# Kernel tuning notes

Measured on AMD Instinct MI355X. Metric: run time of the kernel, lower is better.

## Reference

```python
import jax, jax.numpy as jnp
import numpy as np

DIM = 1024
N_HEADS = 16
HEAD_DIM = DIM // N_HEADS
EPS = 1e-05
ROPE_BASE = 1000000.0


def apply_rope(x, base=ROPE_BASE):
    # x: [b, seq, heads, head_dim]
    b, seq, n_heads, dim = x.shape
    half = dim // 2
    i = jnp.arange(half)
    theta = 1.0 / base ** (2 * i / dim)
    pos = jnp.arange(seq)
    angles = pos[:, None] * theta[None, :]            # [seq, half]
    cos = jnp.cos(angles)[None, :, None, :]           # [1, seq, 1, half]
    sin = jnp.sin(angles)[None, :, None, :]
    x1, x2 = jnp.split(x, 2, axis=-1)
    return jnp.concatenate([x1 * cos - x2 * sin, x1 * sin + x2 * cos], axis=-1)


def setup_inputs() -> dict:
    key = jax.random.key(0)
    ks = jax.random.split(key, 6)
    b, seq = 2, 2048
    scale = 1.0 / np.sqrt(DIM)
    x = jax.random.normal(ks[0], (b, seq, DIM), dtype=jnp.float32)
    w_norm = jnp.ones((DIM,), dtype=jnp.float32)
    Wq = jax.random.normal(ks[1], (DIM, DIM), dtype=jnp.float32) * scale
    Wk = jax.random.normal(ks[2], (DIM, DIM), dtype=jnp.float32) * scale
    Wv = jax.random.normal(ks[3], (DIM, DIM), dtype=jnp.float32) * scale
    Wo = jax.random.normal(ks[4], (DIM, DIM), dtype=jnp.float32) * scale
    return {"x": x, "w_norm": w_norm, "Wq": Wq, "Wk": Wk, "Wv": Wv, "Wo": Wo}


def reference(x, w_norm, Wq, Wk, Wv, Wo):
    b, seq, d = x.shape
    # RMSNorm
    rms = jnp.sqrt(jnp.mean(x * x, axis=-1, keepdims=True) + EPS)
    x_norm = x / rms * w_norm
    # QKV projections (Dense without bias: y = x @ W)
    q = (x_norm @ Wq).reshape(b, seq, N_HEADS, HEAD_DIM)
    k = (x_norm @ Wk).reshape(b, seq, N_HEADS, HEAD_DIM)
    v = (x_norm @ Wv).reshape(b, seq, N_HEADS, HEAD_DIM)
    q = apply_rope(q)
    k = apply_rope(k)
    # Causal attention with full [b,h,t,s] scores (faithful to source)
    scores = jnp.einsum('bthd,bshd->bhts', q, k) / jnp.sqrt(jnp.float32(HEAD_DIM))
    causal = jnp.triu(jnp.full((seq, seq), -jnp.inf, dtype=scores.dtype), k=1)
    scores = scores + causal[None, None, :, :]
    attn = jax.nn.softmax(scores, axis=-1)
    out = jnp.einsum('bhts,bshd->bthd', attn, v).reshape(b, seq, d)
    return out @ Wo
```

## Files before the change

### kernel.cpp

```cpp
#include <hip/hip_runtime.h>

#define DIM 1024
#define SEQ 2048
#define BATCH 2
#define NHEADS 16
#define HD 64
#define ROWS (BATCH * SEQ)

typedef __bf16 bf16x8 __attribute__((ext_vector_type(8)));
typedef __bf16 bf16x4 __attribute__((ext_vector_type(4)));
typedef float f32x4 __attribute__((ext_vector_type(4)));
typedef float f32x16 __attribute__((ext_vector_type(16)));
typedef unsigned u32x4 __attribute__((ext_vector_type(4)));

__device__ __forceinline__ f32x4 f4zero() {
    f32x4 z = {0.f, 0.f, 0.f, 0.f};
    return z;
}

__device__ __forceinline__ unsigned cvtpk(float lo, float hi) {
    unsigned r;
    asm("v_cvt_pk_bf16_f32 %0, %1, %2" : "=v"(r) : "v"(lo), "v"(hi));
    return r;
}

__device__ __forceinline__ void pl32swap(unsigned& a, unsigned& b) {
    asm volatile("v_permlane32_swap_b32 %0, %1" : "+v"(a), "+v"(b));
}

#define GLOAD_LDS16(g, l)                                                                  \
    __builtin_amdgcn_global_load_lds((const __attribute__((address_space(1))) void*)(g),   \
                                     (__attribute__((address_space(3))) void*)(l), 16, 0, 0)

__global__ __launch_bounds__(256) void rmsnorm_bf16(const float* __restrict__ x,
                                                    const float* __restrict__ w,
                                                    __bf16* __restrict__ xn) {
    int row = blockIdx.x;
    int t = threadIdx.x;
    float4 v = ((const float4*)(x + (size_t)row * DIM))[t];
    float ss = v.x * v.x + v.y * v.y + v.z * v.z + v.w * v.w;
#pragma unroll
    for (int off = 1; off < 64; off <<= 1) ss += __shfl_xor(ss, off);
    __shared__ float red[4];
    if ((t & 63) == 0) red[t >> 6] = ss;
    __syncthreads();
    ss = red[0] + red[1] + red[2] + red[3];
    float scale = rsqrtf(ss * (1.0f / DIM) + 1e-5f);
    float4 wv = ((const float4*)w)[t];
    bf16x4 o;
    o[0] = (__bf16)(v.x * scale * wv.x);
    o[1] = (__bf16)(v.y * scale * wv.y);
    o[2] = (__bf16)(v.z * scale * wv.z);
    o[3] = (__bf16)(v.w * scale * wv.w);
    *(bf16x4*)(xn + (size_t)row * DIM + t * 4) = o;
}

__global__ __launch_bounds__(256) void wcvt_kernel(const float* __restrict__ Wq,
                                                   const float* __restrict__ Wk,
                                                   const float* __restrict__ Wv,
                                                   const float* __restrict__ Wo,
                                                   __bf16* tq, __bf16* tk, __bf16* tv, __bf16* to_) {
    int z = blockIdx.z;
    const float* W = z == 0 ? Wq : z == 1 ? Wk : z == 2 ? Wv : Wo;
    __bf16* T = z == 0 ? tq : z == 1 ? tk : z == 2 ? tv : to_;
    __shared__ float tile[32][33];
    int n0 = blockIdx.x * 32, k0 = blockIdx.y * 32;
    int tx = threadIdx.x & 31, ty = threadIdx.x >> 5;
#pragma unroll
    for (int j = 0; j < 32; j += 8) tile[ty + j][tx] = W[(size_t)(k0 + ty + j) * DIM + n0 + tx];
    __syncthreads();
#pragma unroll
    for (int j = 0; j < 32; j += 8)
        T[(size_t)(n0 + ty + j) * DIM + k0 + tx] = (__bf16)tile[tx][ty + j];
}

__global__ __launch_bounds__(256) void rope_table_kernel(float* __restrict__ cosT,
                                                         float* __restrict__ sinT) {
    int idx = blockIdx.x * 256 + threadIdx.x;
    int s = idx >> 5, i = idx & 31;
    float e = (2.0f * (float)i) / 64.0f;
    float theta = 1.0f / powf(1000000.0f, e);
    float ang = (float)s * theta;
    cosT[idx] = cosf(ang);
    sinT[idx] = sinf(ang);
}

__device__ __forceinline__ void gemm_core(const __bf16* __restrict__ A,
                                          const __bf16* __restrict__ Bt,
                                          int K, __bf16* As, __bf16* Bs,
                                          f32x4 (&acc)[4][4], int row0, int col0) {
    int tid = threadIdx.x;
    int w = tid >> 6, l = tid & 63, l15 = l & 15, g = l >> 4;
    int wr = (w >> 1) << 6, wc = (w & 1) << 6;

    int sr0 = tid >> 2;
    int sr1 = 64 + (tid >> 2);
    int lc0 = (((tid & 3) ^ ((tid >> 3) & 3)) << 3);
    const __bf16* gA0 = A + (size_t)(row0 + sr0) * K + lc0;
    const __bf16* gA1 = A + (size_t)(row0 + sr1) * K + lc0;
    const __bf16* gB0 = Bt + (size_t)(col0 + sr0) * K + lc0;
    const __bf16* gB1 = Bt + (size_t)(col0 + sr1) * K + lc0;
    __bf16* lA0 = As + w * 512;
    __bf16* lA1 = As + 2048 + w * 512;
    __bf16* lB0 = Bs + w * 512;
    __bf16* lB1 = Bs + 2048 + w * 512;

    int rca = ((g ^ ((l15 >> 1) & 3)) << 3);

#pragma unroll
    for (int i = 0; i < 4; ++i)
#pragma unroll
        for (int j = 0; j < 4; ++j) acc[i][j] = f4zero();

    for (int k0 = 0; k0 < K; k0 += 32) {
        __syncthreads();
        GLOAD_LDS16(gA0 + k0, lA0);
        GLOAD_LDS16(gA1 + k0, lA1);
        GLOAD_LDS16(gB0 + k0, lB0);
        GLOAD_LDS16(gB1 + k0, lB1);
        __syncthreads();

        bf16x8 af[4], bfr[4];
#pragma unroll
        for (int i = 0; i < 4; ++i) af[i] = *(const bf16x8*)&As[(wr + i * 16 + l15) * 32 + rca];
#pragma unroll
        for (int j = 0; j < 4; ++j) bfr[j] = *(const bf16x8*)&Bs[(wc + j * 16 + l15) * 32 + rca];
        __builtin_amdgcn_s_setprio(1);
#pragma unroll
        for (int i = 0; i < 4; ++i)
#pragma unroll
            for (int j = 0; j < 4; ++j)
                acc[i][j] = __builtin_amdgcn_mfma_f32_16x16x32_bf16(af[i], bfr[j], acc[i][j], 0, 0, 0);
        __builtin_amdgcn_s_setprio(0);
    }
}

__global__ __launch_bounds__(256) void gemm_qkv_kernel(const __bf16* __restrict__ xn,
                                                       const __bf16* __restrict__ wq,
                                                       const __bf16* __restrict__ wk,
                                                       const __bf16* __restrict__ wv,
                                                       __bf16* __restrict__ qo,
                                                       __bf16* __restrict__ ko,
                                                       __bf16* __restrict__ vt,
                                                       const float* __restrict__ cosT,
                                                       const float* __restrict__ sinT) {
    __shared__ __bf16 As[128 * 32];
    __shared__ __bf16 Bs[128 * 32];
    int bid = blockIdx.x;
    int tid = threadIdx.x;
    int w = tid >> 6, l = tid & 63, l15 = l & 15, g = l >> 4;
    int wr = (w >> 1) << 6, wc = (w & 1) << 6;
    f32x4 acc[4][4];

    if (bid < 512) {
        int z = bid >> 8, t = bid & 255;
        int col0 = (t & 7) << 7, row0 = (t >> 3) << 7;
        gemm_core(xn, z ? wk : wq, DIM, As, Bs, acc, row0, col0);
        __bf16* C = z ? ko : qo;
        int colbase = col0 + wc;
#pragma unroll
        for (int i = 0; i < 4; ++i) {
#pragma unroll
            for (int r = 0; r < 4; ++r) {
                int row = row0 + wr + i * 16 + g * 4 + r;
                int s = row & (SEQ - 1);
#pragma unroll
                for (int j = 0; j < 2; ++j) {
                    float c = cosT[s * 32 + j * 16 + l15];
                    float sn = sinT[s * 32 + j * 16 + l15];
                    float x1 = acc[i][j][r], x2 = acc[i][j + 2][r];
                    C[(size_t)row * DIM + colbase + j * 16 + l15] = (__bf16)(x1 * c - x2 * sn);
                    C[(size_t)row * DIM + colbase + (j + 2) * 16 + l15] = (__bf16)(x1 * sn + x2 * c);
                }
            }
        }
    } else {
        int t = bid - 512;
        int b = t >> 7, r7 = t & 127;
        int row0 = (r7 >> 4) << 7;
        int col0 = (r7 & 15) << 7;
        gemm_core(wv, xn + (size_t)b * SEQ * DIM, DIM, As, Bs, acc, row0, col0);
        __bf16* C = vt + (size_t)b * (NHEADS * HD) * SEQ;
#pragma unroll
        for (int i = 0; i < 4; ++i)
#pragma unroll
            for (int j = 0; j < 4; ++j)
#pragma unroll
                for (int r = 0; r < 4; ++r) {
                    int row = row0 + wr + i * 16 + g * 4 + r;
                    int col = col0 + wc + j * 16 + l15;
                    C[(size_t)row * SEQ + col] = (__bf16)acc[i][j][r];
                }
    }
}

__global__ __launch_bounds__(256) void gemm_out_kernel(const __bf16* __restrict__ ctx,
                                                       const __bf16* __restrict__ wo,
                                                       float* __restrict__ out) {
    __shared__ __bf16 As[128 * 32];
    __shared__ __bf16 Bs[128 * 32];
    int row0 = (int)blockIdx.y << 7, col0 = (int)blockIdx.x << 7;
    f32x4 acc[4][4];
    gemm_core(ctx, wo, DIM, As, Bs, acc, row0, col0);
    int tid = threadIdx.x;
    int w = tid >> 6, l = tid & 63, l15 = l & 15, g = l >> 4;
    int wr = (w >> 1) << 6, wc = (w & 1) << 6;
#pragma unroll
    for (int i = 0; i < 4; ++i)
#pragma unroll
        for (int j = 0; j < 4; ++j)
#pragma unroll
            for (int r = 0; r < 4; ++r) {
                int row = row0 + wr + i * 16 + g * 4 + r;
                int col = col0 + wc + j * 16 + l15;
                out[(size_t)row * DIM + col] = acc[i][j][r];
            }
}

__global__ __launch_bounds__(512) void attn_fused_kernel(const __bf16* __restrict__ q,
                                                         const __bf16* __restrict__ k,
                                                         const __bf16* __restrict__ vt,
                                                         __bf16* __restrict__ ctx) {
    int bh = blockIdx.x;
    int qb = blockIdx.y;
    int b = bh >> 4, h = bh & 15;
    __shared__ __bf16 Ks[2][64][72];
    __shared__ __bf16 Vs[2][64][72];
    int tid = threadIdx.x, w = tid >> 6, l = tid & 63;
    int l31 = l & 31, hi = l >> 5;
    size_t hoff = (size_t)(b * SEQ) * DIM + h * HD;
    const __bf16* vth = vt + (size_t)bh * HD * SEQ;
    int qw0 = qb * 256 + w * 32;
    int qrow = qw0 + l31;
    int ntiles = 4 * qb + 4;
    int mytiles = 4 * qb + (w >> 1) + 1;

    bf16x8 qf[4];
    {
        const __bf16* qptr = q + hoff + (size_t)qrow * DIM + hi * 8;
        const float c2 = 0.125f * 1.44269504f;
#pragma unroll
        for (int g = 0; g < 4; ++g) {
            bf16x8 t0 = *(const bf16x8*)(qptr + g * 16);
#pragma unroll
            for (int e = 0; e < 8; ++e) qf[g][e] = (__bf16)((float)t0[e] * c2);
        }
    }

    f32x16 oA, oB;
#pragma unroll
    for (int r = 0; r < 16; ++r) {
        oA[r] = 0.f;
        oB[r] = 0.f;
    }
    float m_run = -1e30f, l_run = 0.f;

    int srow = tid >> 3, scol = (tid & 7) * 8;
    const __bf16* kst = k + hoff + (size_t)srow * DIM + scol;
    const __bf16* vst = vth + (size_t)srow * SEQ + scol;

    bf16x8 kr = *(const bf16x8*)kst;
    bf16x8 vr = *(const bf16x8*)vst;
    *(bf16x8*)&Ks[0][srow][scol] = kr;
    *(bf16x8*)&Vs[0][srow][scol] = vr;
    kr = *(const bf16x8*)(kst + (size_t)64 * DIM);
    vr = *(const bf16x8*)(vst + 64);
    __syncthreads();

    for (int st = 0; st < ntiles; ++st) {
        int cur = st & 1;
        bf16x8 kn, vn;
        if (st + 2 < ntiles) {
            kn = *(const bf16x8*)(kst + (size_t)((st + 2) * 64) * DIM);
            vn = *(const bf16x8*)(vst + (st + 2) * 64);
        }

        if (st < mytiles) {
            int s0 = st << 6;
            f32x16 sa, sb;
#pragma unroll
            for (int r = 0; r < 16; ++r) {
                sa[r] = 0.f;
                sb[r] = 0.f;
            }
            __builtin_amdgcn_s_setprio(1);
#pragma unroll
            for (int g = 0; g < 4; ++g) {
                bf16x8 ka = *(const bf16x8*)&Ks[cur][l31][g * 16 + hi * 8];
                bf16x8 kb2 = *(const bf16x8*)&Ks[cur][32 + l31][g * 16 + hi * 8];
                sa = __builtin_amdgcn_mfma_f32_32x32x16_bf16(ka, qf[g], sa, 0, 0, 0);
                sb = __builtin_amdgcn_mfma_f32_32x32x16_bf16(kb2, qf[g], sb, 0, 0, 0);
            }
            __builtin_amdgcn_s_setprio(0);

            if (s0 + 63 > qw0) {
#pragma unroll
                for (int r = 0; r < 16; ++r) {
                    int kg = s0 + (r & 3) + 8 * (r >> 2) + 4 * hi;
                    if (kg > qrow) sa[r] = -1e30f;
                    if (kg + 32 > qrow) sb[r] = -1e30f;
                }
            }

            float lmax = -3e38f;
#pragma unroll
            for (int r = 0; r < 16; ++r) lmax = fmaxf(lmax, fmaxf(sa[r], sb[r]));
            if (!__all(lmax <= m_run + 10.0f)) {
                float omax = fmaxf(lmax, __shfl_xor(lmax, 32));
                float m_new = fmaxf(m_run, omax);
                float alpha = exp2f(m_run - m_new);
                l_run *= alpha;
#pragma unroll
                for (int r = 0; r < 16; ++r) {
                    oA[r] *= alpha;
                    oB[r] *= alpha;
                }
                m_run = m_new;
            }
            float ls = 0.f;
#pragma unroll
            for (int r = 0; r < 16; ++r) {
                sa[r] = exp2f(sa[r] - m_run);
                ls += sa[r];
                sb[r] = exp2f(sb[r] - m_run);
                ls += sb[r];
            }
            l_run += ls + __shfl_xor(ls, 32);

            bf16x8 pa[4];
#pragma unroll
            for (int g = 0; g < 2; ++g) {
                unsigned a_ = cvtpk(sa[8 * g + 0], sa[8 * g + 1]);
                unsigned b_ = cvtpk(sa[8 * g + 4], sa[8 * g + 5]);
                pl32swap(a_, b_);
                unsigned c_ = cvtpk(sa[8 * g + 2], sa[8 * g + 3]);
                unsigned d_ = cvtpk(sa[8 * g + 6], sa[8 * g + 7]);
                pl32swap(c_, d_);
                u32x4 t4 = {a_, c_, b_, d_};
                pa[g] = __builtin_bit_cast(bf16x8, t4);
            }
#pragma unroll
            for (int g = 0; g < 2; ++g) {
                unsigned a_ = cvtpk(sb[8 * g + 0], sb[8 * g + 1]);
                unsigned b_ = cvtpk(sb[8 * g + 4], sb[8 * g + 5]);
                pl32swap(a_, b_);
                unsigned c_ = cvtpk(sb[8 * g + 2], sb[8 * g + 3]);
                unsigned d_ = cvtpk(sb[8 * g + 6], sb[8 * g + 7]);
                pl32swap(c_, d_);
                u32x4 t4 = {a_, c_, b_, d_};
                pa[2 + g] = __builtin_bit_cast(bf16x8, t4);
            }

            __builtin_amdgcn_s_setprio(1);
#pragma unroll
            for (int ks = 0; ks < 4; ++ks) {
                bf16x8 va = *(const bf16x8*)&Vs[cur][l31][ks * 16 + hi * 8];
                bf16x8 vb2 = *(const bf16x8*)&Vs[cur][32 + l31][ks * 16 + hi * 8];
                oA = __builtin_amdgcn_mfma_f32_32x32x16_bf16(va, pa[ks], oA, 0, 0, 0);
                oB = __builtin_amdgcn_mfma_f32_32x32x16_bf16(vb2, pa[ks], oB, 0, 0, 0);
            }
            __builtin_amdgcn_s_setprio(0);
        }

        if (st + 1 < ntiles) {
            *(bf16x8*)&Ks[cur ^ 1][srow][scol] = kr;
            *(bf16x8*)&Vs[cur ^ 1][srow][scol] = vr;
            kr = kn;
            vr = vn;
        }
        __syncthreads();
    }

    float inv = 1.0f / l_run;
#pragma unroll
    for (int rr = 0; rr < 16; rr += 4) {
        int d = 8 * (rr >> 2) + 4 * hi;
        uint2 pA = {cvtpk(oA[rr] * inv, oA[rr + 1] * inv), cvtpk(oA[rr + 2] * inv, oA[rr + 3] * inv)};
        uint2 pB = {cvtpk(oB[rr] * inv, oB[rr + 1] * inv), cvtpk(oB[rr + 2] * inv, oB[rr + 3] * inv)};
        *(uint2*)&ctx[hoff + (size_t)qrow * DIM + d] = pA;
        *(uint2*)&ctx[hoff + (size_t)qrow * DIM + 32 + d] = pB;
    }
}

extern "C" void kernel_launch(void* const* d_in, const int* in_sizes, int n_in,
                              void* d_out, int out_size, void* d_ws, size_t ws_size,
                              hipStream_t stream) {
    const float* x = (const float*)d_in[0];
    const float* w_norm = (const float*)d_in[1];
    const float* Wq = (const float*)d_in[2];
    const float* Wk = (const float*)d_in[3];
    const float* Wv = (const float*)d_in[4];
    const float* Wo = (const float*)d_in[5];
    float* out = (float*)d_out;
    char* w8 = (char*)d_ws;

    const size_t MB = 1ull << 20;
    __bf16* xn = (__bf16*)(w8);
    __bf16* wtq = (__bf16*)(w8 + 8 * MB);
    __bf16* wtk = (__bf16*)(w8 + 10 * MB);
    __bf16* wtv = (__bf16*)(w8 + 12 * MB);
    __bf16* wto = (__bf16*)(w8 + 14 * MB);
    __bf16* qb = (__bf16*)(w8 + 16 * MB);
    __bf16* kb = (__bf16*)(w8 + 24 * MB);
    __bf16* vtb = (__bf16*)(w8 + 32 * MB);
    __bf16* ctx = (__bf16*)(w8 + 40 * MB);
    float* cosT = (float*)(w8 + 48 * MB);
    float* sinT = cosT + SEQ * 32;

    wcvt_kernel<<<dim3(32, 32, 4), 256, 0, stream>>>(Wq, Wk, Wv, Wo, wtq, wtk, wtv, wto);
    rmsnorm_bf16<<<ROWS, 256, 0, stream>>>(x, w_norm, xn);
    rope_table_kernel<<<(SEQ * 32) / 256, 256, 0, stream>>>(cosT, sinT);

    gemm_qkv_kernel<<<768, 256, 0, stream>>>(xn, wtq, wtk, wtv, qb, kb, vtb, cosT, sinT);

    attn_fused_kernel<<<dim3(BATCH * NHEADS, SEQ / 256), 512, 0, stream>>>(qb, kb, vtb, ctx);

    gemm_out_kernel<<<dim3(DIM / 128, ROWS / 128), 256, 0, stream>>>(ctx, wto, out);
}
```

Before: 144.4 us.

## Rebalance causal attention with 4-wave blocks over interleaved query strips

The attention kernel now uses 256-thread blocks where each wave takes a 32-row query strip spaced 16 strips apart, so every block gets a mix of short and long causal ranges. The blocks are launched in reverse order to even out load across workgroups. Each thread now stages two K/V rows per tile, and the final loop barrier is dropped in favour of an explicit lgkmcnt wait plus s_barrier. Row max and row sum are computed as trees instead of serial chains. The waves in a block still differ a lot in how many tiles they process, so the shared loop runs to the longest strip and some waves sit idle at barriers.

```diff
diff --git a/kernel.cpp b/kernel.cpp
--- a/kernel.cpp
+++ b/kernel.cpp
@@ -217,12 +217,12 @@
             }
 }
 
-__global__ __launch_bounds__(512) void attn_fused_kernel(const __bf16* __restrict__ q,
-                                                         const __bf16* __restrict__ k,
-                                                         const __bf16* __restrict__ vt,
-                                                         __bf16* __restrict__ ctx) {
+__global__ __launch_bounds__(256, 2) void attn_fused_kernel(const __bf16* __restrict__ q,
+                                                            const __bf16* __restrict__ k,
+                                                            const __bf16* __restrict__ vt,
+                                                            __bf16* __restrict__ ctx) {
     int bh = blockIdx.x;
-    int qb = blockIdx.y;
+    int j = 15 - (int)blockIdx.y;
     int b = bh >> 4, h = bh & 15;
     __shared__ __bf16 Ks[2][64][72];
     __shared__ __bf16 Vs[2][64][72];
@@ -230,10 +230,11 @@
     int l31 = l & 31, hi = l >> 5;
     size_t hoff = (size_t)(b * SEQ) * DIM + h * HD;
     const __bf16* vth = vt + (size_t)bh * HD * SEQ;
-    int qw0 = qb * 256 + w * 32;
+    int sidx = j + 16 * w;
+    int qw0 = sidx * 32;
     int qrow = qw0 + l31;
-    int ntiles = 4 * qb + 4;
-    int mytiles = 4 * qb + (w >> 1) + 1;
+    int mytiles = (sidx >> 1) + 1;
+    int ntiles = ((j + 48) >> 1) + 1;
 
     bf16x8 qf[4];
     {
@@ -255,24 +256,35 @@
     }
     float m_run = -1e30f, l_run = 0.f;
 
-    int srow = tid >> 3, scol = (tid & 7) * 8;
-    const __bf16* kst = k + hoff + (size_t)srow * DIM + scol;
-    const __bf16* vst = vth + (size_t)srow * SEQ + scol;
-
-    bf16x8 kr = *(const bf16x8*)kst;
-    bf16x8 vr = *(const bf16x8*)vst;
-    *(bf16x8*)&Ks[0][srow][scol] = kr;
-    *(bf16x8*)&Vs[0][srow][scol] = vr;
-    kr = *(const bf16x8*)(kst + (size_t)64 * DIM);
-    vr = *(const bf16x8*)(vst + 64);
-    __syncthreads();
+    int sr = tid >> 3, sc = (tid & 7) * 8;
+    const __bf16* kst = k + hoff + (size_t)sr * DIM + sc;
+    const __bf16* vst = vth + (size_t)sr * SEQ + sc;
+
+    bf16x8 kr0 = *(const bf16x8*)kst;
+    bf16x8 kr1 = *(const bf16x8*)(kst + (size_t)32 * DIM);
+    bf16x8 vr0 = *(const bf16x8*)vst;
+    bf16x8 vr1 = *(const bf16x8*)(vst + (size_t)32 * SEQ);
+    *(bf16x8*)&Ks[0][sr][sc] = kr0;
+    *(bf16x8*)&Ks[0][32 + sr][sc] = kr1;
+    *(bf16x8*)&Vs[0][sr][sc] = vr0;
+    *(bf16x8*)&Vs[0][32 + sr][sc] = vr1;
+    kr0 = *(const bf16x8*)(kst + (size_t)64 * DIM);
+    kr1 = *(const bf16x8*)(kst + (size_t)96 * DIM);
+    vr0 = *(const bf16x8*)(vst + 64);
+    vr1 = *(const bf16x8*)(vst + (size_t)32 * SEQ + 64);
+    asm volatile("s_waitcnt lgkmcnt(0)" ::: "memory");
+    __builtin_amdgcn_s_barrier();
+    __builtin_amdgcn_sched_barrier(0);
 
     for (int st = 0; st < ntiles; ++st) {
         int cur = st & 1;
-        bf16x8 kn, vn;
+        bf16x8 kn0, kn1, vn0, vn1;
         if (st + 2 < ntiles) {
-            kn = *(const bf16x8*)(kst + (size_t)((st + 2) * 64) * DIM);
-            vn = *(const bf16x8*)(vst + (st + 2) * 64);
+            size_t ko = (size_t)((st + 2) * 64) * DIM;
+            kn0 = *(const bf16x8*)(kst + ko);
+            kn1 = *(const bf16x8*)(kst + ko + (size_t)32 * DIM);
+            vn0 = *(const bf16x8*)(vst + (st + 2) * 64);
+            vn1 = *(const bf16x8*)(vst + (size_t)32 * SEQ + (st + 2) * 64);
         }
 
         if (st < mytiles) {
@@ -302,9 +314,14 @@
                 }
             }
 
-            float lmax = -3e38f;
-#pragma unroll
-            for (int r = 0; r < 16; ++r) lmax = fmaxf(lmax, fmaxf(sa[r], sb[r]));
+            float mx[8];
+#pragma unroll
+            for (int r = 0; r < 8; ++r) mx[r] = fmaxf(sa[r], sa[r + 8]);
+#pragma unroll
+            for (int r = 0; r < 8; ++r) mx[r] = fmaxf(mx[r], fmaxf(sb[r], sb[r + 8]));
+#pragma unroll
+            for (int r = 0; r < 4; ++r) mx[r] = fmaxf(mx[r], mx[r + 4]);
+            float lmax = fmaxf(fmaxf(mx[0], mx[1]), fmaxf(mx[2], mx[3]));
             if (!__all(lmax <= m_run + 10.0f)) {
                 float omax = fmaxf(lmax, __shfl_xor(lmax, 32));
                 float m_new = fmaxf(m_run, omax);
@@ -317,14 +334,17 @@
                 }
                 m_run = m_new;
             }
-            float ls = 0.f;
+            float s4[8];
 #pragma unroll
             for (int r = 0; r < 16; ++r) {
                 sa[r] = exp2f(sa[r] - m_run);
-                ls += sa[r];
                 sb[r] = exp2f(sb[r] - m_run);
-                ls += sb[r];
-            }
+            }
+#pragma unroll
+            for (int r = 0; r < 8; ++r) s4[r] = (sa[r] + sa[r + 8]) + (sb[r] + sb[r + 8]);
+#pragma unroll
+            for (int r = 0; r < 4; ++r) s4[r] += s4[r + 4];
+            float ls = (s4[0] + s4[1]) + (s4[2] + s4[3]);
             l_run += ls + __shfl_xor(ls, 32);
 
             bf16x8 pa[4];
@@ -363,12 +383,18 @@
         }
 
         if (st + 1 < ntiles) {
-            *(bf16x8*)&Ks[cur ^ 1][srow][scol] = kr;
-            *(bf16x8*)&Vs[cur ^ 1][srow][scol] = vr;
-            kr = kn;
-            vr = vn;
+            *(bf16x8*)&Ks[cur ^ 1][sr][sc] = kr0;
+            *(bf16x8*)&Ks[cur ^ 1][32 + sr][sc] = kr1;
+            *(bf16x8*)&Vs[cur ^ 1][sr][sc] = vr0;
+            *(bf16x8*)&Vs[cur ^ 1][32 + sr][sc] = vr1;
+            kr0 = kn0;
+            kr1 = kn1;
+            vr0 = vn0;
+            vr1 = vn1;
+            asm volatile("s_waitcnt lgkmcnt(0)" ::: "memory");
+            __builtin_amdgcn_s_barrier();
+            __builtin_amdgcn_sched_barrier(0);
         }
-        __syncthreads();
     }
 
     float inv = 1.0f / l_run;
@@ -413,7 +439,7 @@
 
     gemm_qkv_kernel<<<768, 256, 0, stream>>>(xn, wtq, wtk, wtv, qb, kb, vtb, cosT, sinT);
 
-    attn_fused_kernel<<<dim3(BATCH * NHEADS, SEQ / 256), 512, 0, stream>>>(qb, kb, vtb, ctx);
+    attn_fused_kernel<<<dim3(BATCH * NHEADS, 16), 256, 0, stream>>>(qb, kb, vtb, ctx);
 
     gemm_out_kernel<<<dim3(DIM / 128, ROWS / 128), 256, 0, stream>>>(ctx, wto, out);
 }
```

Result: faster. 140.1 us (-3.0%).
